# Kernel optimization log

Hardware: AMD Instinct MI355X
Metric: run time of the kernel (lower is better)

Reference implementation:

```python
import jax, jax.numpy as jnp
import numpy as np

B, L, D = 1, 4096, 1024
H, DH = 16, 64
BASE = 10000.0


def _rope_tables(L, dh, dtype=jnp.float32):
    inv_freq = 1.0 / (BASE ** (jnp.arange(0, dh, 2, dtype=jnp.float32) / dh))
    freqs = jnp.outer(jnp.arange(L, dtype=jnp.float32), inv_freq)  # [L, dh/2]
    return jnp.cos(freqs).astype(dtype), jnp.sin(freqs).astype(dtype)


def _apply_rope(x, cos, sin):
    # x: [B,H,L,dh]; cos/sin: [L,dh/2]
    x1, x2 = x[..., ::2], x[..., 1::2]
    c = cos[None, None]
    s = sin[None, None]
    return jnp.concatenate([x1 * c - x2 * s, x1 * s + x2 * c], axis=-1)


def setup_inputs() -> dict:
    key = jax.random.key(0)
    ks = jax.random.split(key, 5)
    x = jax.random.normal(ks[0], (B, L, D), dtype=jnp.float32)
    mask = jnp.tril(jnp.ones((L, L), dtype=jnp.int32))  # causal 0/1 mask
    sd = 1.0 / np.sqrt(D)
    Wq = jax.random.normal(ks[1], (D, D), dtype=jnp.float32) * sd
    Wk = jax.random.normal(ks[2], (D, D), dtype=jnp.float32) * sd
    Wv = jax.random.normal(ks[3], (D, D), dtype=jnp.float32) * sd
    Wo = jax.random.normal(ks[4], (D, D), dtype=jnp.float32) * sd
    return {"x": x, "mask": mask, "Wq": Wq, "Wk": Wk, "Wv": Wv, "Wo": Wo}


def reference(x, mask, Wq, Wk, Wv, Wo):
    b, l, d = x.shape
    scale = DH ** -0.5
    cos, sin = _rope_tables(l, DH, x.dtype)

    def heads(w):
        return (x @ w.T).reshape(b, l, H, DH).transpose(0, 2, 1, 3)  # [B,H,L,dh]

    q = _apply_rope(heads(Wq), cos, sin)
    k = _apply_rope(heads(Wk), cos, sin)
    v = heads(Wv)

    attn = jnp.einsum('bhqd,bhkd->bhqk', q, k) * scale
    attn = jnp.where(mask[:l, :l] == 0, -jnp.inf, attn)
    attn = jax.nn.softmax(attn, axis=-1)
    out = jnp.einsum('bhqk,bhkd->bhqd', attn, v)
    out = out.transpose(0, 2, 1, 3).reshape(b, l, d)
    return out @ Wo.T
```

## Files before the change

### kernel.cpp

```cpp
#include <hip/hip_runtime.h>
#include <math.h>

#define LSEQ   4096
#define DMODEL 1024
#define NH     16
#define DHEAD  64
#define PSTRIDE 40
#define MASKV  -30000.0f
#define C2SCALE 0.18033688f

typedef __attribute__((ext_vector_type(8))) short  bf16x8;
typedef __attribute__((ext_vector_type(4))) float  floatx4;
typedef unsigned short ushort_t;

#if __has_builtin(__builtin_amdgcn_exp2f)
#define EXP2F __builtin_amdgcn_exp2f
#else
#define EXP2F exp2f
#endif

__device__ __forceinline__ ushort_t f2bf(float x) {
  unsigned u = __builtin_bit_cast(unsigned, x);
  return (ushort_t)((u + 0x7fff + ((u >> 16) & 1)) >> 16);
}
__device__ __forceinline__ unsigned bf16pair(float a, float b) {
  return (unsigned)f2bf(a) | ((unsigned)f2bf(b) << 16);
}
__device__ __forceinline__ unsigned bfpack_trunc(float a, float b) {
  return __builtin_amdgcn_perm(__builtin_bit_cast(unsigned, b),
                               __builtin_bit_cast(unsigned, a), 0x07060302u);
}
__device__ __forceinline__ void gl_lds16(const ushort_t* g, ushort_t* l) {
  __builtin_amdgcn_global_load_lds(
      (const __attribute__((address_space(1))) void*)g,
      (__attribute__((address_space(3))) void*)l, 16, 0, 0);
}

__global__ void rope_table(float2* __restrict__ rope) {
  const int idx = blockIdx.x * 256 + threadIdx.x;
  const int s = idx >> 5, t = idx & 31;
  const double invf = exp((double)t * -0.28782313662425572);
  const double ang = (double)s * invf;
  rope[idx] = make_float2((float)cos(ang), (float)sin(ang));
}

__global__ void cvt_bf16(const float* __restrict__ x,  const float* __restrict__ wq,
                         const float* __restrict__ wk, const float* __restrict__ wv,
                         const float* __restrict__ wo, ushort_t* __restrict__ dst) {
  const size_t e = ((size_t)blockIdx.x * 256 + threadIdx.x) * 4;
  const float* src; size_t off;
  if      (e < (size_t)(4u << 20)) { src = x;  off = e; }
  else if (e < (size_t)(5u << 20)) { src = wq; off = e - (size_t)(4u << 20); }
  else if (e < (size_t)(6u << 20)) { src = wk; off = e - (size_t)(5u << 20); }
  else if (e < (size_t)(7u << 20)) { src = wv; off = e - (size_t)(6u << 20); }
  else                             { src = wo; off = e - (size_t)(7u << 20); }
  const float4 v = *(const float4*)(src + off);
  uint2 p; p.x = bf16pair(v.x, v.y); p.y = bf16pair(v.z, v.w);
  *(uint2*)(dst + e) = p;
}

template<int MODE>
__global__ __launch_bounds__(256)
void mfma_gemm(const ushort_t* __restrict__ A, const ushort_t* __restrict__ B,
               float* __restrict__ C, const float2* __restrict__ rope,
               ushort_t* __restrict__ Qo, ushort_t* __restrict__ Ko,
               ushort_t* __restrict__ Vo) {
  __shared__ ushort_t As[128 * 64];
  __shared__ ushort_t Bs[128 * 64];
  const int tid  = threadIdx.x;
  const int w    = tid >> 6, lane = tid & 63;
  const int wm   = w >> 1,   wn   = w & 1;
  const int quad = lane >> 4, col = lane & 15;
  const int i0 = blockIdx.x * 128;
  const int j0 = blockIdx.y * 128;

  const ushort_t* Ab = A + (size_t)i0 * DMODEL;
  const ushort_t* Bb = B + (size_t)j0 * DMODEL;

  floatx4 acc[4][4];
#pragma unroll
  for (int mt = 0; mt < 4; ++mt)
#pragma unroll
    for (int nt = 0; nt < 4; ++nt) acc[mt][nt] = (floatx4){0.f, 0.f, 0.f, 0.f};

  const int lrow = lane >> 3;
  const int lcol = (lane & 7) * 8;

  for (int k0 = 0; k0 < DMODEL; k0 += 64) {
    __syncthreads();
#pragma unroll
    for (int it = 0; it < 4; ++it) {
      const int rb = (it * 4 + w) * 8;
      gl_lds16(Ab + (size_t)(rb + lrow) * DMODEL + k0 + lcol, As + rb * 64);
      gl_lds16(Bb + (size_t)(rb + lrow) * DMODEL + k0 + lcol, Bs + rb * 64);
    }
    __syncthreads();

#pragma unroll
    for (int kk = 0; kk < 64; kk += 32) {
      bf16x8 af[4], bfr[4];
#pragma unroll
      for (int mt = 0; mt < 4; ++mt)
        af[mt] = *(const bf16x8*)(As + (wm * 64 + mt * 16 + col) * 64 + kk + quad * 8);
#pragma unroll
      for (int nt = 0; nt < 4; ++nt)
        bfr[nt] = *(const bf16x8*)(Bs + (wn * 64 + nt * 16 + col) * 64 + kk + quad * 8);
#pragma unroll
      for (int mt = 0; mt < 4; ++mt)
#pragma unroll
        for (int nt = 0; nt < 4; ++nt)
          acc[mt][nt] = __builtin_amdgcn_mfma_f32_16x16x32_bf16(
              af[mt], bfr[nt], acc[mt][nt], 0, 0, 0);
    }
  }

  if (MODE == 0) {
#pragma unroll
    for (int mt = 0; mt < 4; ++mt) {
      const int i = i0 + wm * 64 + mt * 16 + quad * 4;
#pragma unroll
      for (int nt = 0; nt < 4; ++nt) {
        const int j = j0 + wn * 64 + nt * 16 + col;
#pragma unroll
        for (int r = 0; r < 4; ++r)
          C[(size_t)(i + r) * DMODEL + j] = acc[mt][nt][r];
      }
    }
  } else {
    const int which = i0 >> 10;
#pragma unroll
    for (int mt = 0; mt < 4; ++mt) {
      const int f0 = i0 + wm * 64 + mt * 16 + quad * 4;
      const int h  = (f0 >> 6) & 15;
      const int d  = f0 & 63;
      if (which == 2) {
#pragma unroll
        for (int nt = 0; nt < 4; ++nt) {
          const int s = j0 + wn * 64 + nt * 16 + col;
#pragma unroll
          for (int r = 0; r < 4; ++r)
            Vo[(size_t)(h * DHEAD + d + r) * LSEQ + s] = f2bf(acc[mt][nt][r]);
        }
      } else {
        ushort_t* dst = which ? Ko : Qo;
        const float qs = which ? 1.0f : C2SCALE;
        const int t0 = d >> 1;
#pragma unroll
        for (int nt = 0; nt < 4; ++nt) {
          const int s = j0 + wn * 64 + nt * 16 + col;
          const float4 cst = *(const float4*)((const float*)rope + ((size_t)s << 6) + t0 * 2);
          ushort_t* ob = dst + ((size_t)h * LSEQ + s) * DHEAD;
          const float x1 = acc[mt][nt][0], x2 = acc[mt][nt][1];
          const float y1 = acc[mt][nt][2], y2 = acc[mt][nt][3];
          *(unsigned*)(ob + t0)      = bf16pair((x1 * cst.x - x2 * cst.y) * qs,
                                                (y1 * cst.z - y2 * cst.w) * qs);
          *(unsigned*)(ob + t0 + 32) = bf16pair((x1 * cst.y + x2 * cst.x) * qs,
                                                (y1 * cst.w + y2 * cst.z) * qs);
        }
      }
    }
  }
}

__global__ __launch_bounds__(512, 2)
void attn_mfma(const ushort_t* __restrict__ Qh, const ushort_t* __restrict__ Kh,
               const ushort_t* __restrict__ Vt, ushort_t* __restrict__ Om) {
  const int h   = blockIdx.x;
  const int g   = blockIdx.y;
  const int tid = threadIdx.x;
  const int w    = tid >> 6;
  const int wl   = w & 3;
  const int half = w >> 2;
  const int lane = tid & 63;
  const int quad = lane >> 4;
  const int col  = lane & 15;
  const int csw  = col & 7;

  __shared__ __align__(16) char smem[53248];
  ushort_t* Ks   = (ushort_t*)smem;
  ushort_t* Vs   = (ushort_t*)(smem + 16384);
  ushort_t* Ps   = (ushort_t*)(smem + 32768);
  float*    Obuf = (float*)smem;
  __shared__ float lbuf[4][2][16];
  ushort_t* psw = Ps + w * (32 * PSTRIDE);

  const int srow = w * 8 + (lane >> 3);
  const int scol = (((lane & 7) ^ ((lane >> 3) & 7)) * 8);

  for (int pass = 0; pass < 2; ++pass) {
    const int qb      = pass ? (31 - g) : g;
    const int qbase   = qb * 128 + wl * 32;
    const int nkt_max = 2 * qb + 2;

    bf16x8 qf[2][2];
#pragma unroll
    for (int nq = 0; nq < 2; ++nq)
#pragma unroll
      for (int c = 0; c < 2; ++c)
        qf[nq][c] = *(const bf16x8*)(Qh +
            ((size_t)(h * LSEQ + qbase + nq * 16 + col)) * DHEAD + quad * 8 + c * 32);

    floatx4 ot[4][2];
#pragma unroll
    for (int md = 0; md < 4; ++md)
#pragma unroll
      for (int nq = 0; nq < 2; ++nq) ot[md][nq] = (floatx4){0.f, 0.f, 0.f, 0.f};
    float l_[2] = {0.f, 0.f};

    auto stage = [&](int kt, int b) {
      const int key0 = kt * 64;
      gl_lds16(Kh + ((size_t)(h * LSEQ + key0 + srow)) * DHEAD + scol,
               Ks + b * 4096 + w * 512);
      gl_lds16(Vt + ((size_t)(h * DHEAD + srow)) * LSEQ + key0 + scol,
               Vs + b * 4096 + w * 512);
    };

    stage(0, 0);
    __syncthreads();

    for (int kt = 0; kt < nkt_max; ++kt) {
      const int buf = kt & 1;
      if (kt + 1 < nkt_max) stage(kt + 1, buf ^ 1);

      const ushort_t* kb = Ks + buf * 4096;
      const ushort_t* vb = Vs + buf * 4096;

      bf16x8 kf[2][2];
#pragma unroll
      for (int mk = 0; mk < 2; ++mk)
#pragma unroll
        for (int c = 0; c < 2; ++c)
          kf[mk][c] = *(const bf16x8*)(kb + (half * 32 + mk * 16 + col) * 64 +
                                       (((c * 4 + quad) ^ csw) * 8));

      floatx4 st[2][2];
#pragma unroll
      for (int mk = 0; mk < 2; ++mk)
#pragma unroll
        for (int nq = 0; nq < 2; ++nq) st[mk][nq] = (floatx4){0.f, 0.f, 0.f, 0.f};
#pragma unroll
      for (int mk = 0; mk < 2; ++mk)
#pragma unroll
        for (int c = 0; c < 2; ++c)
#pragma unroll
          for (int nq = 0; nq < 2; ++nq)
            st[mk][nq] = __builtin_amdgcn_mfma_f32_16x16x32_bf16(
                kf[mk][c], qf[nq][c], st[mk][nq], 0, 0, 0);

      if (kt >= nkt_max - 2) {
        const int key0 = kt * 64 + half * 32;
#pragma unroll
        for (int mk = 0; mk < 2; ++mk) {
          const int keyb = key0 + mk * 16 + quad * 4;
#pragma unroll
          for (int nq = 0; nq < 2; ++nq) {
            const int q = qbase + nq * 16 + col;
#pragma unroll
            for (int r = 0; r < 4; ++r)
              if (keyb + r > q) st[mk][nq][r] = MASKV;
          }
        }
      }

#pragma unroll
      for (int mk = 0; mk < 2; ++mk)
#pragma unroll
        for (int nq = 0; nq < 2; ++nq) {
#pragma unroll
          for (int r = 0; r < 4; ++r) st[mk][nq][r] = EXP2F(st[mk][nq][r]);
          l_[nq] += (st[mk][nq][0] + st[mk][nq][1]) + (st[mk][nq][2] + st[mk][nq][3]);
        }

#pragma unroll
      for (int mk = 0; mk < 2; ++mk)
#pragma unroll
        for (int nq = 0; nq < 2; ++nq) {
          uint2 pk;
          pk.x = bfpack_trunc(st[mk][nq][0], st[mk][nq][1]);
          pk.y = bfpack_trunc(st[mk][nq][2], st[mk][nq][3]);
          *(uint2*)(psw + (nq * 16 + col) * PSTRIDE + mk * 16 + quad * 4) = pk;
        }
      bf16x8 pf[2];
#pragma unroll
      for (int nq = 0; nq < 2; ++nq)
        pf[nq] = *(const bf16x8*)(psw + (nq * 16 + col) * PSTRIDE + quad * 8);

      bf16x8 vf[4];
#pragma unroll
      for (int md = 0; md < 4; ++md)
        vf[md] = *(const bf16x8*)(vb + (md * 16 + col) * 64 +
                                  (((half * 4 + quad) ^ csw) * 8));
#pragma unroll
      for (int md = 0; md < 4; ++md)
#pragma unroll
        for (int nq = 0; nq < 2; ++nq)
          ot[md][nq] = __builtin_amdgcn_mfma_f32_16x16x32_bf16(
              vf[md], pf[nq], ot[md][nq], 0, 0, 0);

      __syncthreads();
    }

    float lr[2];
#pragma unroll
    for (int nq = 0; nq < 2; ++nq) {
      float ls = l_[nq];
      ls += __shfl_xor(ls, 16);
      ls += __shfl_xor(ls, 32);
      lr[nq] = ls;
    }

    if (half == 1) {
#pragma unroll
      for (int nq = 0; nq < 2; ++nq) {
        if (quad == 0) lbuf[wl][nq][col] = lr[nq];
#pragma unroll
        for (int md = 0; md < 4; ++md)
          *(float4*)(Obuf + ((wl * 2 + nq) * 16 + col) * 68 + md * 16 + quad * 4) =
              (float4){ot[md][nq][0], ot[md][nq][1], ot[md][nq][2], ot[md][nq][3]};
      }
    }
    __syncthreads();

    if (half == 0) {
#pragma unroll
      for (int nq = 0; nq < 2; ++nq) {
        const float inv = 1.0f / (lr[nq] + lbuf[wl][nq][col]);
        const int q = qbase + nq * 16 + col;
#pragma unroll
        for (int md = 0; md < 4; ++md) {
          const float4 ob =
              *(const float4*)(Obuf + ((wl * 2 + nq) * 16 + col) * 68 + md * 16 + quad * 4);
          uint2 pk;
          pk.x = bf16pair((ot[md][nq][0] + ob.x) * inv, (ot[md][nq][1] + ob.y) * inv);
          pk.y = bf16pair((ot[md][nq][2] + ob.z) * inv, (ot[md][nq][3] + ob.w) * inv);
          *(uint2*)(Om + (size_t)q * DMODEL + h * DHEAD + md * 16 + quad * 4) = pk;
        }
      }
    }
    __syncthreads();
  }
}

extern "C" void kernel_launch(void* const* d_in, const int* in_sizes, int n_in,
                              void* d_out, int out_size, void* d_ws, size_t ws_size,
                              hipStream_t stream) {
  const float* x  = (const float*)d_in[0];
  const float* Wq = (const float*)d_in[2];
  const float* Wk = (const float*)d_in[3];
  const float* Wv = (const float*)d_in[4];
  const float* Wo = (const float*)d_in[5];
  float* out = (float*)d_out;

  const size_t M1 = (size_t)1 << 20;
  ushort_t* xb  = (ushort_t*)d_ws;
  ushort_t* Wb  = xb  + 4 * M1;
  ushort_t* wob = Wb  + 3 * M1;
  ushort_t* Qh  = wob + 1 * M1;
  ushort_t* Kh  = Qh  + 4 * M1;
  ushort_t* Vt  = Kh  + 4 * M1;
  ushort_t* Om  = Vt  + 4 * M1;
  float2*   rope = (float2*)(Om + 4 * M1);

  rope_table<<<512, 256, 0, stream>>>(rope);
  cvt_bf16<<<8192, 256, 0, stream>>>(x, Wq, Wk, Wv, Wo, xb);
  mfma_gemm<1><<<dim3(3072 / 128, LSEQ / 128), 256, 0, stream>>>(
      Wb, xb, nullptr, rope, Qh, Kh, Vt);
  attn_mfma<<<dim3(NH, 16), 512, 0, stream>>>(Qh, Kh, Vt, Om);
  mfma_gemm<0><<<dim3(LSEQ / 128, DMODEL / 128), 256, 0, stream>>>(
      Om, wob, out, nullptr, nullptr, nullptr, nullptr);
}
```

Baseline: 269.0 us.

## Split key tiles across two wave groups in attention with 1024-thread blocks

```diff
diff --git a/kernel.cpp b/kernel.cpp
--- a/kernel.cpp
+++ b/kernel.cpp
@@ -162,35 +162,38 @@
   }
 }
 
-__global__ __launch_bounds__(512, 2)
+__global__ __launch_bounds__(1024, 4)
 void attn_mfma(const ushort_t* __restrict__ Qh, const ushort_t* __restrict__ Kh,
                const ushort_t* __restrict__ Vt, ushort_t* __restrict__ Om) {
   const int h   = blockIdx.x;
   const int g   = blockIdx.y;
   const int tid = threadIdx.x;
-  const int w    = tid >> 6;
-  const int wl   = w & 3;
-  const int half = w >> 2;
+  const int w     = tid >> 6;
+  const int wl    = w & 3;
+  const int half  = (w >> 2) & 1;
+  const int ktpar = w >> 3;
+  const int wg    = w & 7;
   const int lane = tid & 63;
   const int quad = lane >> 4;
   const int col  = lane & 15;
   const int csw  = col & 7;
 
-  __shared__ __align__(16) char smem[53248];
+  __shared__ __align__(16) char smem[106496];
   ushort_t* Ks   = (ushort_t*)smem;
-  ushort_t* Vs   = (ushort_t*)(smem + 16384);
-  ushort_t* Ps   = (ushort_t*)(smem + 32768);
+  ushort_t* Vs   = (ushort_t*)(smem + 32768);
+  ushort_t* Ps   = (ushort_t*)(smem + 65536);
   float*    Obuf = (float*)smem;
-  __shared__ float lbuf[4][2][16];
+  __shared__ float lbuf[3][4][2][16];
   ushort_t* psw = Ps + w * (32 * PSTRIDE);
 
-  const int srow = w * 8 + (lane >> 3);
+  const int srow = wg * 8 + (lane >> 3);
   const int scol = (((lane & 7) ^ ((lane >> 3) & 7)) * 8);
 
   for (int pass = 0; pass < 2; ++pass) {
     const int qb      = pass ? (31 - g) : g;
     const int qbase   = qb * 128 + wl * 32;
     const int nkt_max = 2 * qb + 2;
+    const int nt2     = nkt_max >> 1;
 
     bf16x8 qf[2][2];
 #pragma unroll
@@ -209,21 +212,23 @@
 
     auto stage = [&](int kt, int b) {
       const int key0 = kt * 64;
+      const int boff = (ktpar * 2 + b) * 4096;
       gl_lds16(Kh + ((size_t)(h * LSEQ + key0 + srow)) * DHEAD + scol,
-               Ks + b * 4096 + w * 512);
+               Ks + boff + wg * 512);
       gl_lds16(Vt + ((size_t)(h * DHEAD + srow)) * LSEQ + key0 + scol,
-               Vs + b * 4096 + w * 512);
+               Vs + boff + wg * 512);
     };
 
-    stage(0, 0);
-    __syncthreads();
-
-    for (int kt = 0; kt < nkt_max; ++kt) {
-      const int buf = kt & 1;
-      if (kt + 1 < nkt_max) stage(kt + 1, buf ^ 1);
-
-      const ushort_t* kb = Ks + buf * 4096;
-      const ushort_t* vb = Vs + buf * 4096;
+    stage(ktpar, 0);
+    __syncthreads();
+
+    for (int ktt = 0; ktt < nt2; ++ktt) {
+      const int kt  = 2 * ktt + ktpar;
+      const int buf = ktt & 1;
+      if (ktt + 1 < nt2) stage(kt + 2, buf ^ 1);
+
+      const ushort_t* kb = Ks + (ktpar * 2 + buf) * 4096;
+      const ushort_t* vb = Vs + (ktpar * 2 + buf) * 4096;
 
       bf16x8 kf[2][2];
 #pragma unroll
@@ -309,30 +314,36 @@
       lr[nq] = ls;
     }
 
-    if (half == 1) {
+    const int di = ((half << 1) | ktpar) - 1;
+    if (di >= 0) {
 #pragma unroll
       for (int nq = 0; nq < 2; ++nq) {
-        if (quad == 0) lbuf[wl][nq][col] = lr[nq];
+        if (quad == 0) lbuf[di][wl][nq][col] = lr[nq];
 #pragma unroll
         for (int md = 0; md < 4; ++md)
-          *(float4*)(Obuf + ((wl * 2 + nq) * 16 + col) * 68 + md * 16 + quad * 4) =
+          *(float4*)(Obuf + di * 8704 + ((wl * 2 + nq) * 16 + col) * 68 + md * 16 + quad * 4) =
               (float4){ot[md][nq][0], ot[md][nq][1], ot[md][nq][2], ot[md][nq][3]};
       }
     }
     __syncthreads();
 
-    if (half == 0) {
+    if (di < 0) {
 #pragma unroll
       for (int nq = 0; nq < 2; ++nq) {
-        const float inv = 1.0f / (lr[nq] + lbuf[wl][nq][col]);
+        const float inv = 1.0f / (lr[nq] + lbuf[0][wl][nq][col] +
+                                  lbuf[1][wl][nq][col] + lbuf[2][wl][nq][col]);
         const int q = qbase + nq * 16 + col;
 #pragma unroll
         for (int md = 0; md < 4; ++md) {
-          const float4 ob =
-              *(const float4*)(Obuf + ((wl * 2 + nq) * 16 + col) * 68 + md * 16 + quad * 4);
+          const int ob_off = ((wl * 2 + nq) * 16 + col) * 68 + md * 16 + quad * 4;
+          const float4 o0 = *(const float4*)(Obuf + ob_off);
+          const float4 o1 = *(const float4*)(Obuf + 8704 + ob_off);
+          const float4 o2 = *(const float4*)(Obuf + 17408 + ob_off);
           uint2 pk;
-          pk.x = bf16pair((ot[md][nq][0] + ob.x) * inv, (ot[md][nq][1] + ob.y) * inv);
-          pk.y = bf16pair((ot[md][nq][2] + ob.z) * inv, (ot[md][nq][3] + ob.w) * inv);
+          pk.x = bf16pair((ot[md][nq][0] + o0.x + o1.x + o2.x) * inv,
+                          (ot[md][nq][1] + o0.y + o1.y + o2.y) * inv);
+          pk.y = bf16pair((ot[md][nq][2] + o0.z + o1.z + o2.z) * inv,
+                          (ot[md][nq][3] + o0.w + o1.w + o2.w) * inv);
           *(uint2*)(Om + (size_t)q * DMODEL + h * DHEAD + md * 16 + quad * 4) = pk;
         }
       }
@@ -365,7 +376,7 @@
   cvt_bf16<<<8192, 256, 0, stream>>>(x, Wq, Wk, Wv, Wo, xb);
   mfma_gemm<1><<<dim3(3072 / 128, LSEQ / 128), 256, 0, stream>>>(
       Wb, xb, nullptr, rope, Qh, Kh, Vt);
-  attn_mfma<<<dim3(NH, 16), 512, 0, stream>>>(Qh, Kh, Vt, Om);
+  attn_mfma<<<dim3(NH, 16), 1024, 0, stream>>>(Qh, Kh, Vt, Om);
   mfma_gemm<0><<<dim3(LSEQ / 128, DMODEL / 128), 256, 0, stream>>>(
       Om, wob, out, nullptr, nullptr, nullptr, nullptr);
 }
```

After: 257.0 us. -4.5%, faster.
